# Performance work log

Measured on AMD Instinct MI355X. Metric: run time of the kernel, lower is better.

The kernel has to match this reference:

```python
import jax, jax.numpy as jnp
import numpy as np

# Module constants derived from init kwargs:
# factor=3, indices_per_spike=64, index_maximum=19, border_pad=5
FACTOR = 3
IPS = 64            # indices_per_spike
INDEX_MAX = 19
BP = 5              # border_pad == width
CENTER = (INDEX_MAX + BP) * FACTOR          # 72
LO = CENTER - BP * FACTOR                   # 57
HI = CENTER + BP * FACTOR                   # 87
NEW_CENTER = LO                             # 57
ALIGNED_LEN = (IPS + 2 * BP) * FACTOR - 2 * BP * FACTOR  # 192


def setup_inputs() -> dict:
    key = jax.random.key(0)
    K, L = 500000, 220
    spikes_up = jax.random.normal(key, (K, L), dtype=jnp.float32)
    return {"spikes_up": spikes_up}


def reference(spikes_up):
    K, L = spikes_up.shape
    hi = min(HI, L)
    # per-row argmax in search window [LO, hi)
    window = spikes_up[:, LO:hi]                               # (K, hi-LO)
    local_peaks = jnp.argmax(window, axis=1)                   # (K,)
    index_max = local_peaks + LO
    starts = index_max - CENTER + BP * FACTOR                  # (K,)
    ends = starts + ALIGNED_LEN
    in_bounds = (starts >= 0) & (ends <= L)
    # shifted gather with clamped offsets
    safe_starts = jnp.clip(starts, 0, L - ALIGNED_LEN)
    offsets = jnp.arange(ALIGNED_LEN)
    all_indices = jnp.clip(safe_starts[:, None] + offsets[None, :], 0, L - 1)  # (K, 192)
    aligned = jnp.take_along_axis(spikes_up, all_indices, axis=1)              # (K, 192)
    # validity: peak must land exactly at NEW_CENTER and the slice in bounds
    at_center = jnp.argmax(aligned, axis=1) == NEW_CENTER
    valid = at_center & in_bounds
    removed_mask = ~valid
    # strided downsample (every FACTOR-th sample), invalid rows zeroed
    ds_idx = jnp.arange(IPS) * FACTOR
    downsampled = aligned[:, ds_idx]                           # (K, 64)
    spikes_final = jnp.where(valid[:, None], downsampled, jnp.zeros((), spikes_up.dtype))
    return spikes_final, removed_mask
```

## Files before the change

### kernel.cpp

```cpp
#include <hip/hip_runtime.h>
#include <cfloat>

#define LCOLS        220
#define WIN_LO       57
#define WIN_HI       86
#define ALIGNED_LEN_ 192
#define MAX_START    28
#define IPS_         64
#define NEW_CENTER_  57
#define TILE_ROWS    64
#define TILE_WORDS   (TILE_ROWS * LCOLS)

__device__ __forceinline__ void async_copy16(const float* gsrc, float* ldst) {
    __builtin_amdgcn_global_load_lds(
        (const __attribute__((address_space(1))) void*)gsrc,
        (__attribute__((address_space(3))) void*)ldst, 16, 0, 0);
}

__global__ __launch_bounds__(64) void peak_align_tile(
    const float* __restrict__ in,
    float* __restrict__ out_spikes,
    float* __restrict__ out_mask,
    int K)
{
    __shared__ __align__(16) float tile[TILE_WORDS];
    __shared__ int srow[TILE_ROWS];

    const int lane = threadIdx.x;
    const long long base = (long long)blockIdx.x * TILE_ROWS;
    const int rows = (int)(((long long)K - base) < TILE_ROWS ? (K - base) : TILE_ROWS);
    const float* src = in + base * LCOLS;

    const int bytes = rows * (LCOLS * 4);
    const int nfull = bytes >> 10;
    for (int it = 0; it < nfull; ++it) {
        async_copy16(src + (it << 8) + lane * 4, &tile[it << 8]);
    }
    const int rem = bytes - (nfull << 10);
    if (lane * 16 < rem) {
        const float4 v = *(const float4*)(src + (nfull << 8) + lane * 4);
        *(float4*)&tile[(nfull << 8) + lane * 4] = v;
    }
    __syncthreads();

    int  s_val = 0;
    bool valid = false;
    if (lane < rows) {
        const float* row = &tile[lane * LCOLS];

        float bv = -FLT_MAX; int bi = WIN_LO;
        #pragma unroll
        for (int j = 14; j <= 21; ++j) {
            const float4 q = *(const float4*)(row + (j << 2));
            const float qq[4] = {q.x, q.y, q.z, q.w};
            #pragma unroll
            for (int k = 0; k < 4; ++k) {
                const int c = (j << 2) + k;
                if (c >= WIN_LO && c <= WIN_HI && qq[k] > bv) { bv = qq[k]; bi = c; }
            }
        }
        const int  start = bi - WIN_LO;
        const bool in_b  = (start <= MAX_START);
        const int  s     = in_b ? start : MAX_START;

        float av = -FLT_MAX; int ai = -1;
        #pragma unroll 5
        for (int j = 0; j < 55; ++j) {
            const float4 q = *(const float4*)(row + (j << 2));
            const float qq[4] = {q.x, q.y, q.z, q.w};
            #pragma unroll
            for (int k = 0; k < 4; ++k) {
                const int c = (j << 2) + k;
                const bool inr = (unsigned)(c - s) < (unsigned)ALIGNED_LEN_;
                if (inr && qq[k] > av) { av = qq[k]; ai = c; }
            }
        }
        valid = in_b && (ai == s + NEW_CENTER_);
        s_val = s;
    }
    srow[lane] = s_val | (valid ? (1 << 30) : 0);
    __syncthreads();

    for (int rr = 0; rr < rows; ++rr) {
        const int pk = srow[rr];
        const int s  = pk & 0xFFFF;
        const float v = tile[rr * LCOLS + s + 3 * lane];
        out_spikes[(base + rr) * IPS_ + lane] = (pk & (1 << 30)) ? v : 0.0f;
    }
    if (lane < rows) out_mask[base + lane] = valid ? 0.0f : 1.0f;
}

extern "C" void kernel_launch(void* const* d_in, const int* in_sizes, int n_in,
                              void* d_out, int out_size, void* d_ws, size_t ws_size,
                              hipStream_t stream) {
    const float* in = (const float*)d_in[0];
    const int K = in_sizes[0] / LCOLS;

    float* out_spikes = (float*)d_out;
    float* out_mask   = out_spikes + (long long)K * IPS_;

    const int grid = (K + TILE_ROWS - 1) / TILE_ROWS;
    hipLaunchKernelGGL(peak_align_tile, dim3(grid), dim3(TILE_ROWS), 0, stream,
                       in, out_spikes, out_mask, K);
}
```

Before: 636.9 us.

## Split per-row argmax across four waves with shared-memory reduction

Grows each block from one wave to four. The tile load is spread across the waves, and the 192-wide second argmax is split into four column quarters, each scanned by its own wave, then merged in shared memory by wave 0 with a lowest-index tie-break. The output store is also spread over the four waves. This is meant to raise compute parallelism per tile, at the cost of extra barriers, shared-memory scratch and an idle-wave phase during the first window argmax.

```diff
diff --git a/kernel.cpp b/kernel.cpp
--- a/kernel.cpp
+++ b/kernel.cpp
@@ -2,6 +2,7 @@
 #include <cfloat>
 
 #define LCOLS        220
+#define NF4          55
 #define WIN_LO       57
 #define WIN_HI       86
 #define ALIGNED_LEN_ 192
@@ -11,43 +12,48 @@
 #define TILE_ROWS    64
 #define TILE_WORDS   (TILE_ROWS * LCOLS)
 
+__device__ __constant__ int Q_LO[4] = {0, 14, 28, 42};
+__device__ __constant__ int Q_HI[4] = {14, 28, 42, 55};
+
 __device__ __forceinline__ void async_copy16(const float* gsrc, float* ldst) {
     __builtin_amdgcn_global_load_lds(
         (const __attribute__((address_space(1))) void*)gsrc,
         (__attribute__((address_space(3))) void*)ldst, 16, 0, 0);
 }
 
-__global__ __launch_bounds__(64) void peak_align_tile(
+__global__ __launch_bounds__(256, 2) void peak_align_tile(
     const float* __restrict__ in,
     float* __restrict__ out_spikes,
     float* __restrict__ out_mask,
     int K)
 {
     __shared__ __align__(16) float tile[TILE_WORDS];
-    __shared__ int srow[TILE_ROWS];
+    __shared__ int   spack[TILE_ROWS];
+    __shared__ float pval[256];
+    __shared__ int   pidx[256];
+    __shared__ int   rpack[TILE_ROWS];
 
-    const int lane = threadIdx.x;
+    const int t    = threadIdx.x;
+    const int lane = t & 63;
+    const int wave = t >> 6;
     const long long base = (long long)blockIdx.x * TILE_ROWS;
     const int rows = (int)(((long long)K - base) < TILE_ROWS ? (K - base) : TILE_ROWS);
     const float* src = in + base * LCOLS;
 
     const int bytes = rows * (LCOLS * 4);
     const int nfull = bytes >> 10;
-    for (int it = 0; it < nfull; ++it) {
+    for (int it = wave; it < nfull; it += 4) {
         async_copy16(src + (it << 8) + lane * 4, &tile[it << 8]);
     }
     const int rem = bytes - (nfull << 10);
-    if (lane * 16 < rem) {
-        const float4 v = *(const float4*)(src + (nfull << 8) + lane * 4);
-        *(float4*)&tile[(nfull << 8) + lane * 4] = v;
+    if (t * 16 < rem) {
+        const float4 v = *(const float4*)(src + (nfull << 8) + t * 4);
+        *(float4*)&tile[(nfull << 8) + t * 4] = v;
     }
     __syncthreads();
 
-    int  s_val = 0;
-    bool valid = false;
-    if (lane < rows) {
+    if (wave == 1 && lane < rows) {
         const float* row = &tile[lane * LCOLS];
-
         float bv = -FLT_MAX; int bi = WIN_LO;
         #pragma unroll
         for (int j = 14; j <= 21; ++j) {
@@ -61,33 +67,58 @@
         }
         const int  start = bi - WIN_LO;
         const bool in_b  = (start <= MAX_START);
-        const int  s     = in_b ? start : MAX_START;
+        spack[lane] = (in_b ? start : MAX_START) | (in_b ? (1 << 8) : 0);
+    }
+    __syncthreads();
 
-        float av = -FLT_MAX; int ai = -1;
-        #pragma unroll 5
-        for (int j = 0; j < 55; ++j) {
-            const float4 q = *(const float4*)(row + (j << 2));
-            const float qq[4] = {q.x, q.y, q.z, q.w};
-            #pragma unroll
-            for (int k = 0; k < 4; ++k) {
-                const int c = (j << 2) + k;
-                const bool inr = (unsigned)(c - s) < (unsigned)ALIGNED_LEN_;
-                if (inr && qq[k] > av) { av = qq[k]; ai = c; }
+    {
+        float av = -FLT_MAX; int ai = 0x7fffffff;
+        if (lane < rows) {
+            const int  pk = spack[lane];
+            const int  s  = pk & 0xFF;
+            const float* row = &tile[lane * LCOLS];
+            const int jlo = Q_LO[wave], jhi = Q_HI[wave];
+            for (int j = jlo; j < jhi; ++j) {
+                const float4 q = *(const float4*)(row + (j << 2));
+                const float qq[4] = {q.x, q.y, q.z, q.w};
+                #pragma unroll
+                for (int k = 0; k < 4; ++k) {
+                    const int c = (j << 2) + k;
+                    const bool inr = (unsigned)(c - s) < (unsigned)ALIGNED_LEN_;
+                    if (inr && qq[k] > av) { av = qq[k]; ai = c; }
+                }
             }
         }
-        valid = in_b && (ai == s + NEW_CENTER_);
-        s_val = s;
+        pval[t] = av; pidx[t] = ai;
     }
-    srow[lane] = s_val | (valid ? (1 << 30) : 0);
     __syncthreads();
 
-    for (int rr = 0; rr < rows; ++rr) {
-        const int pk = srow[rr];
-        const int s  = pk & 0xFFFF;
-        const float v = tile[rr * LCOLS + s + 3 * lane];
-        out_spikes[(base + rr) * IPS_ + lane] = (pk & (1 << 30)) ? v : 0.0f;
+    if (wave == 0 && lane < rows) {
+        float av = pval[lane];      int ai = pidx[lane];
+        #pragma unroll
+        for (int q = 1; q < 4; ++q) {
+            const float v2 = pval[q * 64 + lane];
+            const int   i2 = pidx[q * 64 + lane];
+            if (v2 > av || (v2 == av && i2 < ai)) { av = v2; ai = i2; }
+        }
+        const int  pk    = spack[lane];
+        const int  s     = pk & 0xFF;
+        const bool in_b  = (pk >> 8) != 0;
+        const bool valid = in_b && (ai == s + NEW_CENTER_);
+        rpack[lane] = s | (valid ? (1 << 30) : 0);
+        out_mask[base + lane] = valid ? 0.0f : 1.0f;
     }
-    if (lane < rows) out_mask[base + lane] = valid ? 0.0f : 1.0f;
+    __syncthreads();
+
+    for (int i = 0; i < 16; ++i) {
+        const int rr = wave * 16 + i;
+        if (rr < rows) {
+            const int pk = rpack[rr];
+            const int s  = pk & 0xFF;
+            const float v = tile[rr * LCOLS + s + 3 * lane];
+            out_spikes[(base + rr) * IPS_ + lane] = (pk & (1 << 30)) ? v : 0.0f;
+        }
+    }
 }
 
 extern "C" void kernel_launch(void* const* d_in, const int* in_sizes, int n_in,
@@ -100,6 +131,6 @@
     float* out_mask   = out_spikes + (long long)K * IPS_;
 
     const int grid = (K + TILE_ROWS - 1) / TILE_ROWS;
-    hipLaunchKernelGGL(peak_align_tile, dim3(grid), dim3(TILE_ROWS), 0, stream,
+    hipLaunchKernelGGL(peak_align_tile, dim3(grid), dim3(256), 0, stream,
                        in, out_spikes, out_mask, K);
 }
```

New measurement: 601.2 us. 1.06x faster.
